# Kernel tuning notes

Hardware: AMD Instinct MI355X
Metric: run time of the kernel (lower is better)

## Reference

```python
import jax, jax.numpy as jnp
import numpy as np

V, N, D, HEADS = 4, 1536, 256, 4


def setup_inputs() -> dict:
    key = jax.random.key(0)
    ks = jax.random.split(key, 8)
    s = 0.05  # weight init scale
    return {
        "H": jax.random.normal(ks[0], (V, N, D), jnp.float32),
        "C": jax.random.normal(ks[1], (V, V, N, N), jnp.float32),
        "WQ": jax.random.normal(ks[2], (V, D, D), jnp.float32) * s,
        "WK": jax.random.normal(ks[3], (V, D, D), jnp.float32) * s,
        "WV": jax.random.normal(ks[4], (V, D, D), jnp.float32) * s,
        "in_proj_w": jax.random.normal(ks[5], (3 * D, D), jnp.float32) * s,
        "in_proj_b": jnp.zeros((3 * D,), jnp.float32),
        "out_proj_w": jax.random.normal(ks[6], (D, D), jnp.float32) * s,
        "out_proj_b": jnp.zeros((D,), jnp.float32),
        "alphas": jnp.full((V,), 0.95, jnp.float32),
        "alpha_align": jnp.asarray(0.5, jnp.float32),
        "beta": jnp.asarray(0.5, jnp.float32),
        "topk": 32,
    }


def _ircva(H, in_proj_w, in_proj_b, out_proj_w, out_proj_b, alphas):
    # torch MultiheadAttention, seq=V, batch=N, embed=D, heads=HEADS
    dh = D // HEADS
    qkv = jnp.einsum('snd,ed->sne', H, in_proj_w) + in_proj_b  # (V,N,3D)
    q, k, v = jnp.split(qkv, 3, axis=-1)
    q = q.reshape(V, N, HEADS, dh)
    k = k.reshape(V, N, HEADS, dh)
    v = v.reshape(V, N, HEADS, dh)
    att = jnp.einsum('snhd,tnhd->nhst', q, k) / jnp.sqrt(jnp.float32(dh))
    w = jax.nn.softmax(att, axis=-1)
    o = jnp.einsum('nhst,tnhd->snhd', w, v).reshape(V, N, D)
    fusion = jnp.einsum('snd,ed->sne', o, out_proj_w) + out_proj_b
    a = alphas[:, None, None]
    return fusion * a + (1.0 - a) * H  # (V,N,D)


def _crcva(aligned, C, WQ, WK, WV, K):
    # per-view projections: Linear y = x @ W.T
    Qn = jnp.einsum('vnd,ved->vne', aligned, WQ)
    Kn = jnp.einsum('vnd,ved->vne', aligned, WK)
    Vn = jnp.einsum('vnd,ved->vne', aligned, WV)
    # per-row top-k sparsification of C[p,q]
    vals, idx = jax.lax.top_k(C, K)  # (V,V,N,K)
    Cf = C.reshape(-1, N)
    rows = jnp.arange(Cf.shape[0])[:, None]
    sparse = jnp.zeros_like(Cf).at[rows, idx.reshape(-1, K)].set(vals.reshape(-1, K))
    sparse = sparse.reshape(V, V, N, N)
    row_sum = sparse.sum(axis=-1, keepdims=True) + 1e-12
    C_hat = sparse / row_sum
    # diagonal (p==q) pairs are left as zeros in the torch code
    offdiag = (1.0 - jnp.eye(V, dtype=C.dtype))[:, :, None, None]
    C_hat = C_hat * offdiag
    mask = (C_hat > 0).astype(C.dtype)
    scores = jnp.einsum('pnd,qmd->pqnm', Qn, Kn) / jnp.sqrt(jnp.float32(D))
    scores = scores * mask + (1.0 - mask) * (-1e9)
    alpha_nbr = jax.nn.softmax(scores, axis=-1)
    return jnp.einsum('pqnm,qmd->pnd', alpha_nbr, Vn)  # (V,N,D)


def reference(H, C, WQ, WK, WV, in_proj_w, in_proj_b, out_proj_w, out_proj_b,
              alphas, alpha_align, beta, topk):
    aligned = _ircva(H, in_proj_w, in_proj_b, out_proj_w, out_proj_b, alphas)
    nbr = _crcva(aligned, C, WQ, WK, WV, int(topk))
    a = jax.nn.sigmoid(alpha_align)
    f_fuse = jax.nn.relu(a * aligned + (1.0 - a) * nbr)
    return beta * H + (1.0 - beta) * f_fuse  # (V,N,D)
```

## Files before the change

### kernel.cpp

```cpp
#include <hip/hip_runtime.h>
#include <hip/hip_bf16.h>
#include <math.h>

typedef __bf16 bf16x8 __attribute__((ext_vector_type(8)));
typedef __bf16 bf16x4 __attribute__((ext_vector_type(4)));
typedef float  f32x4  __attribute__((ext_vector_type(4)));

static constexpr int kV = 4;
static constexpr int kN = 1536;
static constexpr int kD = 256;
static constexpr int kTopK = 32;

__global__ __launch_bounds__(256) void convert_kernel(
    const float* __restrict__ H, const float* __restrict__ inW,
    const float* __restrict__ outW, const float* __restrict__ WQ,
    const float* __restrict__ WK, const float* __restrict__ WV,
    __bf16* __restrict__ Hb, __bf16* __restrict__ inWb,
    __bf16* __restrict__ outWb, __bf16* __restrict__ Wqkvb,
    float* __restrict__ Vmean)
{
    if (blockIdx.x == 0) {
        f32x4 z = {0.f, 0.f, 0.f, 0.f};
        *(f32x4*)(Vmean + threadIdx.x * 4) = z;
    }
    int idx = (blockIdx.x * 256 + threadIdx.x) * 4;
    const float* src; __bf16* dst; int off;
    if      (idx < 1572864) { src = H;    dst = Hb;             off = idx; }
    else if (idx < 1769472) { src = inW;  dst = inWb;           off = idx - 1572864; }
    else if (idx < 1835008) { src = outW; dst = outWb;          off = idx - 1769472; }
    else if (idx < 2097152) { src = WQ;   dst = Wqkvb;          off = idx - 1835008; }
    else if (idx < 2359296) { src = WK;   dst = Wqkvb + 262144; off = idx - 2097152; }
    else                    { src = WV;   dst = Wqkvb + 524288; off = idx - 2359296; }
    f32x4 v = *(const f32x4*)(src + off);
    bf16x4 b;
#pragma unroll
    for (int j = 0; j < 4; ++j) b[j] = (__bf16)v[j];
    *(bf16x4*)(dst + off) = b;
}

__global__ __launch_bounds__(256) void gemm_qkv_kernel(
    const __bf16* __restrict__ A, const __bf16* __restrict__ Bm,
    const float* __restrict__ bias, __bf16* __restrict__ outB)
{
    const int Nc = 768, K = 256;
    int wave = blockIdx.x * 4 + (threadIdx.x >> 6);
    int tm  = wave / 12;
    int tn4 = wave - tm * 12;
    int lane = threadIdx.x & 63;
    int r    = lane & 15;
    int quad = lane >> 4;
    const __bf16* Ap = A + (size_t)(tm * 32 + r) * K + quad * 8;
    const __bf16* Bp = Bm + (size_t)(tn4 * 64 + r) * K + quad * 8;
    f32x4 acc[2][4] = {};
    for (int k0 = 0; k0 < K; k0 += 32) {
        bf16x8 a0 = *(const bf16x8*)(Ap + k0);
        bf16x8 a1 = *(const bf16x8*)(Ap + (size_t)16 * K + k0);
#pragma unroll
        for (int t = 0; t < 4; ++t) {
            bf16x8 b = *(const bf16x8*)(Bp + (size_t)t * 16 * K + k0);
            acc[0][t] = __builtin_amdgcn_mfma_f32_16x16x32_bf16(a0, b, acc[0][t], 0, 0, 0);
            acc[1][t] = __builtin_amdgcn_mfma_f32_16x16x32_bf16(a1, b, acc[1][t], 0, 0, 0);
        }
    }
#pragma unroll
    for (int t = 0; t < 4; ++t) {
        int gn = tn4 * 64 + t * 16 + r;
        float bv = bias[gn];
#pragma unroll
        for (int mt = 0; mt < 2; ++mt)
#pragma unroll
            for (int i = 0; i < 4; ++i) {
                int gm = tm * 32 + mt * 16 + quad * 4 + i;
                outB[(size_t)gm * Nc + gn] = (__bf16)(acc[mt][t][i] + bv);
            }
    }
}

__global__ __launch_bounds__(256) void attg3_kernel(
    const __bf16* __restrict__ qkv, const __bf16* __restrict__ outWb,
    const float* __restrict__ outBias, const float* __restrict__ H,
    const float* __restrict__ alphas,
    float* __restrict__ alignedF, __bf16* __restrict__ alignedB)
{
    __shared__ __bf16 obuf[16][280];
    int n0 = blockIdx.x * 4;
    int tid = threadIdx.x;
    int h = tid >> 6, d = tid & 63;
#pragma unroll
    for (int ni = 0; ni < 4; ++ni) {
        int n = n0 + ni;
        float q[4], k[4], vv[4];
#pragma unroll
        for (int s = 0; s < 4; ++s) {
            size_t base = (size_t)(s * kN + n) * 768 + h * 64 + d;
            q[s]  = (float)qkv[base];
            k[s]  = (float)qkv[base + 256];
            vv[s] = (float)qkv[base + 512];
        }
        float att[4][4];
#pragma unroll
        for (int s = 0; s < 4; ++s)
#pragma unroll
            for (int t = 0; t < 4; ++t) {
                float p = q[s] * k[t];
#pragma unroll
                for (int off = 32; off > 0; off >>= 1) p += __shfl_xor(p, off);
                att[s][t] = p * 0.125f;
            }
#pragma unroll
        for (int s = 0; s < 4; ++s) {
            float mx = fmaxf(fmaxf(att[s][0], att[s][1]), fmaxf(att[s][2], att[s][3]));
            float e0 = __expf(att[s][0] - mx), e1 = __expf(att[s][1] - mx);
            float e2 = __expf(att[s][2] - mx), e3 = __expf(att[s][3] - mx);
            float inv = 1.f / (e0 + e1 + e2 + e3);
            float ov = (e0 * vv[0] + e1 * vv[1] + e2 * vv[2] + e3 * vv[3]) * inv;
            obuf[s * 4 + ni][h * 64 + d] = (__bf16)ov;
        }
    }
    __syncthreads();
    int w = tid >> 6, lane = tid & 63;
    int r = lane & 15, quad = lane >> 4;
    f32x4 acc[4] = {};
    for (int k0 = 0; k0 < 256; k0 += 32) {
        bf16x8 a = *(const bf16x8*)&obuf[r][quad * 8 + k0];
#pragma unroll
        for (int t = 0; t < 4; ++t) {
            bf16x8 b = *(const bf16x8*)(outWb + (size_t)(w * 64 + t * 16 + r) * 256 + quad * 8 + k0);
            acc[t] = __builtin_amdgcn_mfma_f32_16x16x32_bf16(a, b, acc[t], 0, 0, 0);
        }
    }
#pragma unroll
    for (int t = 0; t < 4; ++t) {
        int gn = w * 64 + t * 16 + r;
        float bv = outBias[gn];
#pragma unroll
        for (int i = 0; i < 4; ++i) {
            int rl = quad * 4 + i;
            int s = rl >> 2, ni = rl & 3;
            size_t gr = (size_t)(s * kN + n0 + ni);
            float a_ = alphas[s];
            size_t off = gr * kD + gn;
            float res = a_ * (acc[t][i] + bv) + (1.f - a_) * H[off];
            alignedF[off] = res;
            alignedB[off] = (__bf16)res;
        }
    }
}

__global__ __launch_bounds__(256) void gemm_qkv3_kernel(
    const __bf16* __restrict__ A, const __bf16* __restrict__ W,
    __bf16* __restrict__ Qn, float* __restrict__ KnF, float* __restrict__ VnF,
    float* __restrict__ Vmean)
{
    int proj = blockIdx.y;
    const __bf16* Wb = W + (size_t)proj * 4 * 65536;
    int b = blockIdx.x;
    int view = b / 48;
    int tn4 = threadIdx.x >> 6;
    int lane = threadIdx.x & 63;
    int r = lane & 15, quad = lane >> 4;
    const __bf16* Ap = A + (size_t)(b * 32 + r) * kD + quad * 8;
    const __bf16* Bp = Wb + (size_t)view * 65536 + (size_t)(tn4 * 64 + r) * kD + quad * 8;
    f32x4 acc[2][4] = {};
    for (int k0 = 0; k0 < kD; k0 += 32) {
        bf16x8 a0 = *(const bf16x8*)(Ap + k0);
        bf16x8 a1 = *(const bf16x8*)(Ap + (size_t)16 * kD + k0);
#pragma unroll
        for (int t = 0; t < 4; ++t) {
            bf16x8 bb = *(const bf16x8*)(Bp + (size_t)t * 16 * kD + k0);
            acc[0][t] = __builtin_amdgcn_mfma_f32_16x16x32_bf16(a0, bb, acc[0][t], 0, 0, 0);
            acc[1][t] = __builtin_amdgcn_mfma_f32_16x16x32_bf16(a1, bb, acc[1][t], 0, 0, 0);
        }
    }
    float* OF = (proj == 1) ? KnF : VnF;
#pragma unroll
    for (int t = 0; t < 4; ++t) {
        int gn = tn4 * 64 + t * 16 + r;
#pragma unroll
        for (int mt = 0; mt < 2; ++mt)
#pragma unroll
            for (int i = 0; i < 4; ++i) {
                int gm = b * 32 + mt * 16 + quad * 4 + i;
                if (proj == 0) Qn[(size_t)gm * kD + gn] = (__bf16)acc[mt][t][i];
                else           OF[(size_t)gm * kD + gn] = acc[mt][t][i];
            }
    }
    if (proj == 2) {
#pragma unroll
        for (int t = 0; t < 4; ++t) {
            float cs = 0.f;
#pragma unroll
            for (int mt = 0; mt < 2; ++mt)
#pragma unroll
                for (int i = 0; i < 4; ++i) cs += acc[mt][t][i];
            cs += __shfl_xor(cs, 16);
            cs += __shfl_xor(cs, 32);
            if (quad == 0)
                atomicAdd(&Vmean[view * kD + tn4 * 64 + t * 16 + r], cs * (1.f / 1536.f));
        }
    }
}

__global__ __launch_bounds__(256) void crcva_kernel(
    const float* __restrict__ C,
    const __bf16* __restrict__ Qn, const float* __restrict__ KnF,
    const float* __restrict__ VnF, const float* __restrict__ Vmean,
    const float* __restrict__ alignedF, const float* __restrict__ H,
    const float* __restrict__ alpha_align, const float* __restrict__ beta,
    float* __restrict__ out)
{
    int gid = blockIdx.x;
    int j8  = gid & 7;
    int p   = j8 & 3;
    int n   = ((gid >> 3) << 1) | (j8 >> 2);
    int tid = threadIdx.x;
    int w = tid >> 6, lane = tid & 63;
    __shared__ unsigned int hist[3][257];
    __shared__ unsigned int sbin[3];
    __shared__ unsigned int idxl[3][kTopK];
    __shared__ unsigned int scnt[3];
    __shared__ unsigned int ckey[3][152];
    __shared__ unsigned int cidx[3][152];
    __shared__ float qsh[kD];
    __shared__ float wsh[96];
    __shared__ int   osh[96];
    __shared__ float part[4][kD];

    size_t eoff = ((size_t)p * kN + n) * kD + tid;
    float pre_al = alignedF[eoff];
    float pre_h  = H[eoff];
    float pre_vm = Vmean[p * kD + tid];
    float pre_aa = alpha_align[0];
    float pre_bt = beta[0];

    if (w < 3) {
        int q = w + (w >= p ? 1 : 0);
        const float* row = C + ((size_t)((p * kV + q) * kN + n)) * kN;
        unsigned int key[24];
#pragma unroll
        for (int j = 0; j < 6; ++j) {
            f32x4 v4 = __builtin_nontemporal_load((const f32x4*)(row + j * 256 + lane * 4));
#pragma unroll
            for (int e = 0; e < 4; ++e) {
                unsigned int u = __float_as_uint(v4[e]);
                key[j * 4 + e] = u ^ ((unsigned int)((int)u >> 31) | 0x80000000u);
            }
        }
        if (lane == 0) scnt[w] = 0;
        const unsigned int T0 = 0xBFCCCCCDu;
        unsigned int cand = 0;
#pragma unroll
        for (int j = 0; j < 24; ++j) cand |= (key[j] > T0) ? (1u << j) : 0u;
        unsigned int myc = (unsigned int)__popc(cand);
#pragma unroll
        for (int off = 1; off < 64; off <<= 1) myc += __shfl_xor(myc, off);
        bool fastsel = (myc >= kTopK && myc <= 150);
        unsigned int pref = 0, need = kTopK, h3win = 0;
        unsigned long long below = (1ull << lane) - 1ull;
        if (fastsel) {
            unsigned int ccnt = 0;
#pragma unroll
            for (int j = 0; j < 24; ++j) {
                bool b = (cand >> j) & 1u;
                unsigned long long m = __ballot(b);
                if (b) {
                    unsigned int pos = ccnt + (unsigned int)__popcll(m & below);
                    ckey[w][pos] = key[j];
                    cidx[w][pos] = (unsigned int)((j >> 2) * 256 + lane * 4 + (j & 3));
                }
                ccnt += (unsigned int)__popcll(m);
            }
            __builtin_amdgcn_wave_barrier();
#pragma unroll
            for (int pass = 0; pass < 4; ++pass) {
                const int shift = 24 - 8 * pass;
#pragma unroll
                for (int k2 = 0; k2 < 4; ++k2) hist[w][lane * 4 + k2] = 0;
                __builtin_amdgcn_wave_barrier();
#pragma unroll
                for (int s = 0; s < 3; ++s) {
                    int i = lane + s * 64;
                    if (i < (int)ccnt) {
                        unsigned int k = ckey[w][i];
                        if (pass == 0 || ((k ^ pref) >> (shift + 8)) == 0)
                            atomicAdd(&hist[w][(k >> shift) & 255u], 1u);
                    }
                }
                __builtin_amdgcn_wave_barrier();
                unsigned int h0 = hist[w][lane*4+0], h1 = hist[w][lane*4+1];
                unsigned int h2 = hist[w][lane*4+2], h3 = hist[w][lane*4+3];
                unsigned int s3 = h3, s2 = h2 + s3, s1 = h1 + s2, s0 = h0 + s1;
                unsigned int run = s0;
#pragma unroll
                for (int off = 1; off < 64; off <<= 1) {
                    unsigned int v = __shfl_down(run, off);
                    if (lane + off < 64) run += v;
                }
                unsigned int above = run - s0;
                unsigned int suf[4]  = {above+s0, above+s1, above+s2, above+s3};
                unsigned int sufN[4] = {above+s1, above+s2, above+s3, above};
#pragma unroll
                for (int k2 = 0; k2 < 4; ++k2)
                    if (suf[k2] >= need && sufN[k2] < need)
                        sbin[w] = ((unsigned int)(lane*4 + k2) << 22)
                                | ((suf[k2] - sufN[k2]) << 11) | sufN[k2];
                __builtin_amdgcn_wave_barrier();
                unsigned int pk = sbin[w];
                pref |= (pk >> 22) << shift;
                need -= (pk & 0x7FFu);
                if (pass == 3) h3win = (pk >> 11) & 0x7FFu;
                __builtin_amdgcn_wave_barrier();
            }
            unsigned int T = pref;
            if (h3win == need) {
#pragma unroll
                for (int s = 0; s < 3; ++s) {
                    int i = lane + s * 64;
                    if (i < (int)ccnt && ckey[w][i] >= T) {
                        unsigned int pos = atomicAdd(&scnt[w], 1u);
                        idxl[w][pos] = cidx[w][i];
                    }
                }
            } else {
                unsigned int eqBefore = 0;
                for (int j4 = 0; j4 < 6; ++j4) {
                    unsigned long long m[4];
#pragma unroll
                    for (int e = 0; e < 4; ++e)
                        m[e] = __ballot(((cand >> (j4*4+e)) & 1u) && key[j4*4+e] == T);
#pragma unroll
                    for (int e = 0; e < 4; ++e) {
                        unsigned int k = key[j4 * 4 + e];
                        bool inc = (cand >> (j4*4+e)) & 1u;
                        unsigned int rank = eqBefore;
#pragma unroll
                        for (int e2 = 0; e2 < 4; ++e2) rank += (unsigned int)__popcll(m[e2] & below);
                        for (int e2 = 0; e2 < e; ++e2) rank += (unsigned int)((m[e2] >> lane) & 1ull);
                        bool take = (inc && k > T) || (inc && k == T && rank < need);
                        if (take) {
                            unsigned int pos = atomicAdd(&scnt[w], 1u);
                            idxl[w][pos] = (unsigned int)(j4 * 256 + lane * 4 + e);
                        }
                    }
                    eqBefore += (unsigned int)(__popcll(m[0]) + __popcll(m[1])
                                             + __popcll(m[2]) + __popcll(m[3]));
                }
            }
        } else {
            if (myc < kTopK) {
                cand = 0;
#pragma unroll
                for (int j = 0; j < 24; ++j) cand |= (key[j] > 0x80000000u) ? (1u << j) : 0u;
            }
            need = kTopK;
#pragma unroll
            for (int pass = 0; pass < 4; ++pass) {
                const int shift = 24 - 8 * pass;
#pragma unroll
                for (int k2 = 0; k2 < 4; ++k2) hist[w][lane * 4 + k2] = 0;
                __builtin_amdgcn_wave_barrier();
#pragma unroll
                for (int j = 0; j < 24; ++j) {
                    unsigned int k = key[j];
                    bool match = ((cand >> j) & 1u) &&
                                 ((pass == 0) || (((k ^ pref) >> (shift + 8)) == 0));
                    if (match) atomicAdd(&hist[w][(k >> shift) & 255u], 1u);
                }
                __builtin_amdgcn_wave_barrier();
                unsigned int h0 = hist[w][lane*4+0], h1 = hist[w][lane*4+1];
                unsigned int h2 = hist[w][lane*4+2], h3 = hist[w][lane*4+3];
                unsigned int s3 = h3, s2 = h2 + s3, s1 = h1 + s2, s0 = h0 + s1;
                unsigned int run = s0;
#pragma unroll
                for (int off = 1; off < 64; off <<= 1) {
                    unsigned int v = __shfl_down(run, off);
                    if (lane + off < 64) run += v;
                }
                if (pass == 0) {
                    unsigned int tot = __shfl(run, 0);
                    need = need < tot ? need : tot;
                }
                unsigned int above = run - s0;
                unsigned int suf[4]  = {above+s0, above+s1, above+s2, above+s3};
                unsigned int sufN[4] = {above+s1, above+s2, above+s3, above};
#pragma unroll
                for (int k2 = 0; k2 < 4; ++k2)
                    if (suf[k2] >= need && sufN[k2] < need)
                        sbin[w] = ((unsigned int)(lane*4 + k2) << 22)
                                | ((suf[k2] - sufN[k2]) << 11) | sufN[k2];
                __builtin_amdgcn_wave_barrier();
                unsigned int pk = sbin[w];
                pref |= (pk >> 22) << shift;
                need -= (pk & 0x7FFu);
                if (pass == 3) h3win = (pk >> 11) & 0x7FFu;
                __builtin_amdgcn_wave_barrier();
            }
            unsigned int T = pref;
            if (h3win == need) {
#pragma unroll
                for (int j = 0; j < 24; ++j) {
                    if (((cand >> j) & 1u) && key[j] >= T) {
                        unsigned int pos = atomicAdd(&scnt[w], 1u);
                        idxl[w][pos] = (unsigned int)((j >> 2) * 256 + lane * 4 + (j & 3));
                    }
                }
            } else {
                unsigned int eqBefore = 0;
                for (int j4 = 0; j4 < 6; ++j4) {
                    unsigned long long m[4];
#pragma unroll
                    for (int e = 0; e < 4; ++e)
                        m[e] = __ballot(((cand >> (j4*4+e)) & 1u) && key[j4*4+e] == T);
#pragma unroll
                    for (int e = 0; e < 4; ++e) {
                        unsigned int k = key[j4 * 4 + e];
                        bool inc = (cand >> (j4*4+e)) & 1u;
                        unsigned int rank = eqBefore;
#pragma unroll
                        for (int e2 = 0; e2 < 4; ++e2) rank += (unsigned int)__popcll(m[e2] & below);
                        for (int e2 = 0; e2 < e; ++e2) rank += (unsigned int)((m[e2] >> lane) & 1ull);
                        bool take = (inc && k > T) || (inc && k == T && rank < need);
                        if (take) {
                            unsigned int pos = atomicAdd(&scnt[w], 1u);
                            idxl[w][pos] = (unsigned int)(j4 * 256 + lane * 4 + e);
                        }
                    }
                    eqBefore += (unsigned int)(__popcll(m[0]) + __popcll(m[1])
                                             + __popcll(m[2]) + __popcll(m[3]));
                }
            }
        }
    } else {
        bf16x4 qv = *(const bf16x4*)(Qn + ((size_t)p * kN + n) * kD + lane * 4);
#pragma unroll
        for (int e = 0; e < 4; ++e) qsh[lane * 4 + e] = (float)qv[e];
    }
    __syncthreads();

    if (tid < 192) {
        int j = tid >> 1, half = tid & 1;
        int g = j >> 5, r = j & 31;
        int q = g + (g >= p ? 1 : 0);
        int cnt = (int)scnt[g];
        bool valid = (r < cnt);
        int m = valid ? (int)idxl[g][r] : 0;
        int off = valid ? (q * kN + m) * kD : 0;
        float s = 0.f;
        if (valid) {
            const float* kr = KnF + off + half * 128;
            const float* qh = qsh + half * 128;
            float a0 = 0.f, a1 = 0.f, a2 = 0.f, a3 = 0.f;
#pragma unroll
            for (int dd = 0; dd < 128; dd += 16) {
                f32x4 k0 = *(const f32x4*)(kr + dd);
                f32x4 k1 = *(const f32x4*)(kr + dd + 4);
                f32x4 k2 = *(const f32x4*)(kr + dd + 8);
                f32x4 k3 = *(const f32x4*)(kr + dd + 12);
                const float* q0 = qh + dd;
                a0 += q0[0]*k0[0] + q0[1]*k0[1] + q0[2]*k0[2] + q0[3]*k0[3];
                a1 += q0[4]*k1[0] + q0[5]*k1[1] + q0[6]*k1[2] + q0[7]*k1[3];
                a2 += q0[8]*k2[0] + q0[9]*k2[1] + q0[10]*k2[2] + q0[11]*k2[3];
                a3 += q0[12]*k3[0] + q0[13]*k3[1] + q0[14]*k3[2] + q0[15]*k3[3];
            }
            s = (a0 + a1) + (a2 + a3);
        }
        s += __shfl_xor(s, 1);
        float sc = valid ? s * 0.0625f : -1e30f;
        float mx = sc;
#pragma unroll
        for (int o2 = 2; o2 <= 32; o2 <<= 1) mx = fmaxf(mx, __shfl_xor(mx, o2));
        float e = valid ? __expf(sc - mx) : 0.f;
        float ss = e;
#pragma unroll
        for (int o2 = 2; o2 <= 32; o2 <<= 1) ss += __shfl_xor(ss, o2);
        if (half == 0) {
            wsh[j] = (ss > 0.f) ? e / ss : 0.f;
            osh[j] = off;
        }
    }
    __syncthreads();

    {
        float a0 = 0.f, a1 = 0.f, a2 = 0.f, a3 = 0.f;
#pragma unroll
        for (int jj = 0; jj < 24; ++jj) {
            int j = w * 24 + jj;
            float wt = wsh[j];
            f32x4 v = *(const f32x4*)(VnF + osh[j] + lane * 4);
            a0 += wt * v[0]; a1 += wt * v[1]; a2 += wt * v[2]; a3 += wt * v[3];
        }
        f32x4 av = {a0, a1, a2, a3};
        *(f32x4*)&part[w][lane * 4] = av;
    }
    __syncthreads();

    float acc = pre_vm + part[0][tid] + part[1][tid] + part[2][tid] + part[3][tid];
    float aa = 1.f / (1.f + __expf(-pre_aa));
    float f  = fmaxf(aa * pre_al + (1.f - aa) * acc, 0.f);
    out[eoff] = pre_h * pre_bt + (1.f - pre_bt) * f;
}

extern "C" void kernel_launch(void* const* d_in, const int* in_sizes, int n_in,
                              void* d_out, int out_size, void* d_ws, size_t ws_size,
                              hipStream_t stream)
{
    const float* H        = (const float*)d_in[0];
    const float* C        = (const float*)d_in[1];
    const float* WQ       = (const float*)d_in[2];
    const float* WK       = (const float*)d_in[3];
    const float* WV       = (const float*)d_in[4];
    const float* inW      = (const float*)d_in[5];
    const float* inB      = (const float*)d_in[6];
    const float* outW     = (const float*)d_in[7];
    const float* outBias  = (const float*)d_in[8];
    const float* alphas   = (const float*)d_in[9];
    const float* alpha_al = (const float*)d_in[10];
    const float* beta     = (const float*)d_in[11];
    float* out = (float*)d_out;

    char* w = (char*)d_ws;
    __bf16* Hb       = (__bf16*)w;  w += (size_t)6144 * 256 * 2;
    __bf16* inWb     = (__bf16*)w;  w += (size_t)768 * 256 * 2;
    __bf16* outWb    = (__bf16*)w;  w += (size_t)256 * 256 * 2;
    __bf16* Wqkvb    = (__bf16*)w;  w += (size_t)3 * 4 * 256 * 256 * 2;
    __bf16* qkv      = (__bf16*)w;  w += (size_t)6144 * 768 * 2;
    __bf16* alignedB = (__bf16*)w;  w += (size_t)6144 * 256 * 2;
    float*  alignedF = (float*)w;   w += (size_t)6144 * 256 * 4;
    __bf16* Qn       = (__bf16*)w;  w += (size_t)6144 * 256 * 2;
    float*  KnF      = (float*)w;   w += (size_t)6144 * 256 * 4;
    float*  VnF      = (float*)w;   w += (size_t)6144 * 256 * 4;
    float*  Vmean    = (float*)w;   w += (size_t)4 * 256 * 4;

    convert_kernel<<<2560, 256, 0, stream>>>(H, inW, outW, WQ, WK, WV,
                                             Hb, inWb, outWb, Wqkvb, Vmean);
    gemm_qkv_kernel<<<576, 256, 0, stream>>>(Hb, inWb, inB, qkv);
    attg3_kernel<<<384, 256, 0, stream>>>(qkv, outWb, outBias, H, alphas,
                                          alignedF, alignedB);
    gemm_qkv3_kernel<<<dim3(192, 3), 256, 0, stream>>>(alignedB, Wqkvb,
                                                       Qn, KnF, VnF, Vmean);
    crcva_kernel<<<6144, 256, 0, stream>>>(C, Qn, KnF, VnF, Vmean,
        alignedF, H, alpha_al, beta, out);
}
```

Before: 431.3 us.

## Store K and V projections in bf16 and scope top-k key registers

The K and V projection outputs are now written as bf16 rather than fp32, so the sparse neighbour gather in crcva reads half the bytes per row. The V accumulation is reorganised so each half-wave loads 8 bf16 values and the two halves are combined with a shuffle. The top-k selection code is restructured so the key register array lives in a narrower scope, and the tie-handling slow path reloads the C row from memory instead of keeping the keys live, which may lower register pressure. In exchange, K and V lose precision, and the rare tie path pays for an extra global read.

Measured after the change: 347.5 us. 1.24x faster.

```diff
diff --git a/kernel.cpp b/kernel.cpp
--- a/kernel.cpp
+++ b/kernel.cpp
@@ -149,10 +149,11 @@
 
 __global__ __launch_bounds__(256) void gemm_qkv3_kernel(
     const __bf16* __restrict__ A, const __bf16* __restrict__ W,
-    __bf16* __restrict__ Qn, float* __restrict__ KnF, float* __restrict__ VnF,
+    __bf16* __restrict__ O0, __bf16* __restrict__ O1, __bf16* __restrict__ O2,
     float* __restrict__ Vmean)
 {
     int proj = blockIdx.y;
+    __bf16* Ob = (proj == 0) ? O0 : (proj == 1) ? O1 : O2;
     const __bf16* Wb = W + (size_t)proj * 4 * 65536;
     int b = blockIdx.x;
     int view = b / 48;
@@ -172,7 +173,6 @@
             acc[1][t] = __builtin_amdgcn_mfma_f32_16x16x32_bf16(a1, bb, acc[1][t], 0, 0, 0);
         }
     }
-    float* OF = (proj == 1) ? KnF : VnF;
 #pragma unroll
     for (int t = 0; t < 4; ++t) {
         int gn = tn4 * 64 + t * 16 + r;
@@ -181,8 +181,7 @@
 #pragma unroll
             for (int i = 0; i < 4; ++i) {
                 int gm = b * 32 + mt * 16 + quad * 4 + i;
-                if (proj == 0) Qn[(size_t)gm * kD + gn] = (__bf16)acc[mt][t][i];
-                else           OF[(size_t)gm * kD + gn] = acc[mt][t][i];
+                Ob[(size_t)gm * kD + gn] = (__bf16)acc[mt][t][i];
             }
     }
     if (proj == 2) {
@@ -203,8 +202,8 @@
 
 __global__ __launch_bounds__(256) void crcva_kernel(
     const float* __restrict__ C,
-    const __bf16* __restrict__ Qn, const float* __restrict__ KnF,
-    const float* __restrict__ VnF, const float* __restrict__ Vmean,
+    const __bf16* __restrict__ Qn, const __bf16* __restrict__ Kn,
+    const __bf16* __restrict__ Vn, const float* __restrict__ Vmean,
     const float* __restrict__ alignedF, const float* __restrict__ H,
     const float* __restrict__ alpha_align, const float* __restrict__ beta,
     float* __restrict__ out)
@@ -236,197 +235,203 @@
     if (w < 3) {
         int q = w + (w >= p ? 1 : 0);
         const float* row = C + ((size_t)((p * kV + q) * kN + n)) * kN;
-        unsigned int key[24];
-#pragma unroll
-        for (int j = 0; j < 6; ++j) {
-            f32x4 v4 = __builtin_nontemporal_load((const f32x4*)(row + j * 256 + lane * 4));
-#pragma unroll
-            for (int e = 0; e < 4; ++e) {
-                unsigned int u = __float_as_uint(v4[e]);
-                key[j * 4 + e] = u ^ ((unsigned int)((int)u >> 31) | 0x80000000u);
-            }
-        }
         if (lane == 0) scnt[w] = 0;
         const unsigned int T0 = 0xBFCCCCCDu;
-        unsigned int cand = 0;
-#pragma unroll
-        for (int j = 0; j < 24; ++j) cand |= (key[j] > T0) ? (1u << j) : 0u;
-        unsigned int myc = (unsigned int)__popc(cand);
-#pragma unroll
-        for (int off = 1; off < 64; off <<= 1) myc += __shfl_xor(myc, off);
-        bool fastsel = (myc >= kTopK && myc <= 150);
+        unsigned long long below = (1ull << lane) - 1ull;
         unsigned int pref = 0, need = kTopK, h3win = 0;
-        unsigned long long below = (1ull << lane) - 1ull;
-        if (fastsel) {
-            unsigned int ccnt = 0;
-#pragma unroll
-            for (int j = 0; j < 24; ++j) {
-                bool b = (cand >> j) & 1u;
-                unsigned long long m = __ballot(b);
-                if (b) {
-                    unsigned int pos = ccnt + (unsigned int)__popcll(m & below);
-                    ckey[w][pos] = key[j];
-                    cidx[w][pos] = (unsigned int)((j >> 2) * 256 + lane * 4 + (j & 3));
-                }
-                ccnt += (unsigned int)__popcll(m);
+        unsigned int cand, myc;
+        {
+            unsigned int key[24];
+#pragma unroll
+            for (int j = 0; j < 6; ++j) {
+                f32x4 v4 = __builtin_nontemporal_load((const f32x4*)(row + j * 256 + lane * 4));
+#pragma unroll
+                for (int e = 0; e < 4; ++e) {
+                    unsigned int u = __float_as_uint(v4[e]);
+                    key[j * 4 + e] = u ^ ((unsigned int)((int)u >> 31) | 0x80000000u);
+                }
             }
-            __builtin_amdgcn_wave_barrier();
-#pragma unroll
-            for (int pass = 0; pass < 4; ++pass) {
-                const int shift = 24 - 8 * pass;
-#pragma unroll
-                for (int k2 = 0; k2 < 4; ++k2) hist[w][lane * 4 + k2] = 0;
+            cand = 0;
+#pragma unroll
+            for (int j = 0; j < 24; ++j) cand |= (key[j] > T0) ? (1u << j) : 0u;
+            myc = (unsigned int)__popc(cand);
+#pragma unroll
+            for (int off = 1; off < 64; off <<= 1) myc += __shfl_xor(myc, off);
+            if (myc >= kTopK && myc <= 150) {
+                unsigned int ccnt = 0;
+#pragma unroll
+                for (int j = 0; j < 24; ++j) {
+                    bool b = (cand >> j) & 1u;
+                    unsigned long long m = __ballot(b);
+                    if (b) {
+                        unsigned int pos = ccnt + (unsigned int)__popcll(m & below);
+                        ckey[w][pos] = key[j];
+                        cidx[w][pos] = (unsigned int)((j >> 2) * 256 + lane * 4 + (j & 3));
+                    }
+                    ccnt += (unsigned int)__popcll(m);
+                }
                 __builtin_amdgcn_wave_barrier();
 #pragma unroll
-                for (int s = 0; s < 3; ++s) {
-                    int i = lane + s * 64;
-                    if (i < (int)ccnt) {
-                        unsigned int k = ckey[w][i];
-                        if (pass == 0 || ((k ^ pref) >> (shift + 8)) == 0)
-                            atomicAdd(&hist[w][(k >> shift) & 255u], 1u);
-                    }
-                }
-                __builtin_amdgcn_wave_barrier();
-                unsigned int h0 = hist[w][lane*4+0], h1 = hist[w][lane*4+1];
-                unsigned int h2 = hist[w][lane*4+2], h3 = hist[w][lane*4+3];
-                unsigned int s3 = h3, s2 = h2 + s3, s1 = h1 + s2, s0 = h0 + s1;
-                unsigned int run = s0;
-#pragma unroll
-                for (int off = 1; off < 64; off <<= 1) {
-                    unsigned int v = __shfl_down(run, off);
-                    if (lane + off < 64) run += v;
-                }
-                unsigned int above = run - s0;
-                unsigned int suf[4]  = {above+s0, above+s1, above+s2, above+s3};
-                unsigned int sufN[4] = {above+s1, above+s2, above+s3, above};
-#pragma unroll
-                for (int k2 = 0; k2 < 4; ++k2)
-                    if (suf[k2] >= need && sufN[k2] < need)
-                        sbin[w] = ((unsigned int)(lane*4 + k2) << 22)
-                                | ((suf[k2] - sufN[k2]) << 11) | sufN[k2];
-                __builtin_amdgcn_wave_barrier();
-                unsigned int pk = sbin[w];
-                pref |= (pk >> 22) << shift;
-                need -= (pk & 0x7FFu);
-                if (pass == 3) h3win = (pk >> 11) & 0x7FFu;
-                __builtin_amdgcn_wave_barrier();
-            }
-            unsigned int T = pref;
-            if (h3win == need) {
-#pragma unroll
-                for (int s = 0; s < 3; ++s) {
-                    int i = lane + s * 64;
-                    if (i < (int)ccnt && ckey[w][i] >= T) {
-                        unsigned int pos = atomicAdd(&scnt[w], 1u);
-                        idxl[w][pos] = cidx[w][i];
+                for (int pass = 0; pass < 4; ++pass) {
+                    const int shift = 24 - 8 * pass;
+#pragma unroll
+                    for (int k2 = 0; k2 < 4; ++k2) hist[w][lane * 4 + k2] = 0;
+                    __builtin_amdgcn_wave_barrier();
+#pragma unroll
+                    for (int s = 0; s < 3; ++s) {
+                        int i = lane + s * 64;
+                        if (i < (int)ccnt) {
+                            unsigned int k = ckey[w][i];
+                            if (pass == 0 || ((k ^ pref) >> (shift + 8)) == 0)
+                                atomicAdd(&hist[w][(k >> shift) & 255u], 1u);
+                        }
+                    }
+                    __builtin_amdgcn_wave_barrier();
+                    unsigned int h0 = hist[w][lane*4+0], h1 = hist[w][lane*4+1];
+                    unsigned int h2 = hist[w][lane*4+2], h3 = hist[w][lane*4+3];
+                    unsigned int s3 = h3, s2 = h2 + s3, s1 = h1 + s2, s0 = h0 + s1;
+                    unsigned int run = s0;
+#pragma unroll
+                    for (int off = 1; off < 64; off <<= 1) {
+                        unsigned int v = __shfl_down(run, off);
+                        if (lane + off < 64) run += v;
+                    }
+                    unsigned int above = run - s0;
+                    unsigned int suf[4]  = {above+s0, above+s1, above+s2, above+s3};
+                    unsigned int sufN[4] = {above+s1, above+s2, above+s3, above};
+#pragma unroll
+                    for (int k2 = 0; k2 < 4; ++k2)
+                        if (suf[k2] >= need && sufN[k2] < need)
+                            sbin[w] = ((unsigned int)(lane*4 + k2) << 22)
+                                    | ((suf[k2] - sufN[k2]) << 11) | sufN[k2];
+                    __builtin_amdgcn_wave_barrier();
+                    unsigned int pk = sbin[w];
+                    pref |= (pk >> 22) << shift;
+                    need -= (pk & 0x7FFu);
+                    if (pass == 3) h3win = (pk >> 11) & 0x7FFu;
+                    __builtin_amdgcn_wave_barrier();
+                }
+                unsigned int T = pref;
+                if (h3win == need) {
+#pragma unroll
+                    for (int s = 0; s < 3; ++s) {
+                        int i = lane + s * 64;
+                        if (i < (int)ccnt && ckey[w][i] >= T) {
+                            unsigned int pos = atomicAdd(&scnt[w], 1u);
+                            idxl[w][pos] = cidx[w][i];
+                        }
+                    }
+                } else {
+                    unsigned int eqBefore = 0;
+                    for (int j4 = 0; j4 < 6; ++j4) {
+                        unsigned int k4[4];
+                        f32x4 v4 = *(const f32x4*)(row + j4 * 256 + lane * 4);
+#pragma unroll
+                        for (int e = 0; e < 4; ++e) {
+                            unsigned int u = __float_as_uint(v4[e]);
+                            k4[e] = u ^ ((unsigned int)((int)u >> 31) | 0x80000000u);
+                        }
+                        unsigned long long m[4];
+#pragma unroll
+                        for (int e = 0; e < 4; ++e) m[e] = __ballot(k4[e] == T);
+#pragma unroll
+                        for (int e = 0; e < 4; ++e) {
+                            unsigned int k = k4[e];
+                            unsigned int rank = eqBefore;
+#pragma unroll
+                            for (int e2 = 0; e2 < 4; ++e2) rank += (unsigned int)__popcll(m[e2] & below);
+                            for (int e2 = 0; e2 < e; ++e2) rank += (unsigned int)((m[e2] >> lane) & 1ull);
+                            bool take = (k > T) || (k == T && rank < need);
+                            if (take) {
+                                unsigned int pos = atomicAdd(&scnt[w], 1u);
+                                idxl[w][pos] = (unsigned int)(j4 * 256 + lane * 4 + e);
+                            }
+                        }
+                        eqBefore += (unsigned int)(__popcll(m[0]) + __popcll(m[1])
+                                                 + __popcll(m[2]) + __popcll(m[3]));
                     }
                 }
             } else {
-                unsigned int eqBefore = 0;
-                for (int j4 = 0; j4 < 6; ++j4) {
-                    unsigned long long m[4];
-#pragma unroll
-                    for (int e = 0; e < 4; ++e)
-                        m[e] = __ballot(((cand >> (j4*4+e)) & 1u) && key[j4*4+e] == T);
-#pragma unroll
-                    for (int e = 0; e < 4; ++e) {
-                        unsigned int k = key[j4 * 4 + e];
-                        bool inc = (cand >> (j4*4+e)) & 1u;
-                        unsigned int rank = eqBefore;
-#pragma unroll
-                        for (int e2 = 0; e2 < 4; ++e2) rank += (unsigned int)__popcll(m[e2] & below);
-                        for (int e2 = 0; e2 < e; ++e2) rank += (unsigned int)((m[e2] >> lane) & 1ull);
-                        bool take = (inc && k > T) || (inc && k == T && rank < need);
-                        if (take) {
+                if (myc < kTopK) {
+                    cand = 0;
+#pragma unroll
+                    for (int j = 0; j < 24; ++j) cand |= (key[j] > 0x80000000u) ? (1u << j) : 0u;
+                }
+#pragma unroll
+                for (int pass = 0; pass < 4; ++pass) {
+                    const int shift = 24 - 8 * pass;
+#pragma unroll
+                    for (int k2 = 0; k2 < 4; ++k2) hist[w][lane * 4 + k2] = 0;
+                    __builtin_amdgcn_wave_barrier();
+#pragma unroll
+                    for (int j = 0; j < 24; ++j) {
+                        unsigned int k = key[j];
+                        bool match = ((cand >> j) & 1u) &&
+                                     ((pass == 0) || (((k ^ pref) >> (shift + 8)) == 0));
+                        if (match) atomicAdd(&hist[w][(k >> shift) & 255u], 1u);
+                    }
+                    __builtin_amdgcn_wave_barrier();
+                    unsigned int h0 = hist[w][lane*4+0], h1 = hist[w][lane*4+1];
+                    unsigned int h2 = hist[w][lane*4+2], h3 = hist[w][lane*4+3];
+                    unsigned int s3 = h3, s2 = h2 + s3, s1 = h1 + s2, s0 = h0 + s1;
+                    unsigned int run = s0;
+#pragma unroll
+                    for (int off = 1; off < 64; off <<= 1) {
+                        unsigned int v = __shfl_down(run, off);
+                        if (lane + off < 64) run += v;
+                    }
+                    if (pass == 0) {
+                        unsigned int tot = __shfl(run, 0);
+                        need = need < tot ? need : tot;
+                    }
+                    unsigned int above = run - s0;
+                    unsigned int suf[4]  = {above+s0, above+s1, above+s2, above+s3};
+                    unsigned int sufN[4] = {above+s1, above+s2, above+s3, above};
+#pragma unroll
+                    for (int k2 = 0; k2 < 4; ++k2)
+                        if (suf[k2] >= need && sufN[k2] < need)
+                            sbin[w] = ((unsigned int)(lane*4 + k2) << 22)
+                                    | ((suf[k2] - sufN[k2]) << 11) | sufN[k2];
+                    __builtin_amdgcn_wave_barrier();
+                    unsigned int pk = sbin[w];
+                    pref |= (pk >> 22) << shift;
+                    need -= (pk & 0x7FFu);
+                    if (pass == 3) h3win = (pk >> 11) & 0x7FFu;
+                    __builtin_amdgcn_wave_barrier();
+                }
+                unsigned int T = pref;
+                if (h3win == need) {
+#pragma unroll
+                    for (int j = 0; j < 24; ++j) {
+                        if (((cand >> j) & 1u) && key[j] >= T) {
                             unsigned int pos = atomicAdd(&scnt[w], 1u);
-                            idxl[w][pos] = (unsigned int)(j4 * 256 + lane * 4 + e);
+                            idxl[w][pos] = (unsigned int)((j >> 2) * 256 + lane * 4 + (j & 3));
                         }
                     }
-                    eqBefore += (unsigned int)(__popcll(m[0]) + __popcll(m[1])
-                                             + __popcll(m[2]) + __popcll(m[3]));
-                }
-            }
-        } else {
-            if (myc < kTopK) {
-                cand = 0;
-#pragma unroll
-                for (int j = 0; j < 24; ++j) cand |= (key[j] > 0x80000000u) ? (1u << j) : 0u;
-            }
-            need = kTopK;
-#pragma unroll
-            for (int pass = 0; pass < 4; ++pass) {
-                const int shift = 24 - 8 * pass;
-#pragma unroll
-                for (int k2 = 0; k2 < 4; ++k2) hist[w][lane * 4 + k2] = 0;
-                __builtin_amdgcn_wave_barrier();
-#pragma unroll
-                for (int j = 0; j < 24; ++j) {
-                    unsigned int k = key[j];
-                    bool match = ((cand >> j) & 1u) &&
-                                 ((pass == 0) || (((k ^ pref) >> (shift + 8)) == 0));
-                    if (match) atomicAdd(&hist[w][(k >> shift) & 255u], 1u);
-                }
-                __builtin_amdgcn_wave_barrier();
-                unsigned int h0 = hist[w][lane*4+0], h1 = hist[w][lane*4+1];
-                unsigned int h2 = hist[w][lane*4+2], h3 = hist[w][lane*4+3];
-                unsigned int s3 = h3, s2 = h2 + s3, s1 = h1 + s2, s0 = h0 + s1;
-                unsigned int run = s0;
-#pragma unroll
-                for (int off = 1; off < 64; off <<= 1) {
-                    unsigned int v = __shfl_down(run, off);
-                    if (lane + off < 64) run += v;
-                }
-                if (pass == 0) {
-                    unsigned int tot = __shfl(run, 0);
-                    need = need < tot ? need : tot;
-                }
-                unsigned int above = run - s0;
-                unsigned int suf[4]  = {above+s0, above+s1, above+s2, above+s3};
-                unsigned int sufN[4] = {above+s1, above+s2, above+s3, above};
-#pragma unroll
-                for (int k2 = 0; k2 < 4; ++k2)
-                    if (suf[k2] >= need && sufN[k2] < need)
-                        sbin[w] = ((unsigned int)(lane*4 + k2) << 22)
-                                | ((suf[k2] - sufN[k2]) << 11) | sufN[k2];
-                __builtin_amdgcn_wave_barrier();
-                unsigned int pk = sbin[w];
-                pref |= (pk >> 22) << shift;
-                need -= (pk & 0x7FFu);
-                if (pass == 3) h3win = (pk >> 11) & 0x7FFu;
-                __builtin_amdgcn_wave_barrier();
-            }
-            unsigned int T = pref;
-            if (h3win == need) {
-#pragma unroll
-                for (int j = 0; j < 24; ++j) {
-                    if (((cand >> j) & 1u) && key[j] >= T) {
-                        unsigned int pos = atomicAdd(&scnt[w], 1u);
-                        idxl[w][pos] = (unsigned int)((j >> 2) * 256 + lane * 4 + (j & 3));
-                    }
-                }
-            } else {
-                unsigned int eqBefore = 0;
-                for (int j4 = 0; j4 < 6; ++j4) {
-                    unsigned long long m[4];
-#pragma unroll
-                    for (int e = 0; e < 4; ++e)
-                        m[e] = __ballot(((cand >> (j4*4+e)) & 1u) && key[j4*4+e] == T);
-#pragma unroll
-                    for (int e = 0; e < 4; ++e) {
-                        unsigned int k = key[j4 * 4 + e];
-                        bool inc = (cand >> (j4*4+e)) & 1u;
-                        unsigned int rank = eqBefore;
-#pragma unroll
-                        for (int e2 = 0; e2 < 4; ++e2) rank += (unsigned int)__popcll(m[e2] & below);
-                        for (int e2 = 0; e2 < e; ++e2) rank += (unsigned int)((m[e2] >> lane) & 1ull);
-                        bool take = (inc && k > T) || (inc && k == T && rank < need);
-                        if (take) {
-                            unsigned int pos = atomicAdd(&scnt[w], 1u);
-                            idxl[w][pos] = (unsigned int)(j4 * 256 + lane * 4 + e);
+                } else {
+                    unsigned int eqBefore = 0;
+                    for (int j4 = 0; j4 < 6; ++j4) {
+                        unsigned long long m[4];
+#pragma unroll
+                        for (int e = 0; e < 4; ++e)
+                            m[e] = __ballot(((cand >> (j4*4+e)) & 1u) && key[j4*4+e] == T);
+#pragma unroll
+                        for (int e = 0; e < 4; ++e) {
+                            unsigned int k = key[j4 * 4 + e];
+                            bool inc = (cand >> (j4*4+e)) & 1u;
+                            unsigned int rank = eqBefore;
+#pragma unroll
+                            for (int e2 = 0; e2 < 4; ++e2) rank += (unsigned int)__popcll(m[e2] & below);
+                            for (int e2 = 0; e2 < e; ++e2) rank += (unsigned int)((m[e2] >> lane) & 1ull);
+                            bool take = (inc && k > T) || (inc && k == T && rank < need);
+                            if (take) {
+                                unsigned int pos = atomicAdd(&scnt[w], 1u);
+                                idxl[w][pos] = (unsigned int)(j4 * 256 + lane * 4 + e);
+                            }
                         }
-                    }
-                    eqBefore += (unsigned int)(__popcll(m[0]) + __popcll(m[1])
-                                             + __popcll(m[2]) + __popcll(m[3]));
+                        eqBefore += (unsigned int)(__popcll(m[0]) + __popcll(m[1])
+                                                 + __popcll(m[2]) + __popcll(m[3]));
+                    }
                 }
             }
         }
@@ -447,20 +452,23 @@
         int off = valid ? (q * kN + m) * kD : 0;
         float s = 0.f;
         if (valid) {
-            const float* kr = KnF + off + half * 128;
-            const float* qh = qsh + half * 128;
+            const __bf16* kr = Kn + off + half * 128;
+            const float*  qh = qsh + half * 128;
             float a0 = 0.f, a1 = 0.f, a2 = 0.f, a3 = 0.f;
 #pragma unroll
-            for (int dd = 0; dd < 128; dd += 16) {
-                f32x4 k0 = *(const f32x4*)(kr + dd);
-                f32x4 k1 = *(const f32x4*)(kr + dd + 4);
-                f32x4 k2 = *(const f32x4*)(kr + dd + 8);
-                f32x4 k3 = *(const f32x4*)(kr + dd + 12);
+            for (int dd = 0; dd < 128; dd += 32) {
+                bf16x8 k0 = *(const bf16x8*)(kr + dd);
+                bf16x8 k1 = *(const bf16x8*)(kr + dd + 8);
+                bf16x8 k2 = *(const bf16x8*)(kr + dd + 16);
+                bf16x8 k3 = *(const bf16x8*)(kr + dd + 24);
                 const float* q0 = qh + dd;
-                a0 += q0[0]*k0[0] + q0[1]*k0[1] + q0[2]*k0[2] + q0[3]*k0[3];
-                a1 += q0[4]*k1[0] + q0[5]*k1[1] + q0[6]*k1[2] + q0[7]*k1[3];
-                a2 += q0[8]*k2[0] + q0[9]*k2[1] + q0[10]*k2[2] + q0[11]*k2[3];
-                a3 += q0[12]*k3[0] + q0[13]*k3[1] + q0[14]*k3[2] + q0[15]*k3[3];
+#pragma unroll
+                for (int e = 0; e < 8; ++e) {
+                    a0 += q0[e]      * (float)k0[e];
+                    a1 += q0[e + 8]  * (float)k1[e];
+                    a2 += q0[e + 16] * (float)k2[e];
+                    a3 += q0[e + 24] * (float)k3[e];
+                }
             }
             s = (a0 + a1) + (a2 + a3);
         }
@@ -481,16 +489,22 @@
     __syncthreads();
 
     {
-        float a0 = 0.f, a1 = 0.f, a2 = 0.f, a3 = 0.f;
-#pragma unroll
-        for (int jj = 0; jj < 24; ++jj) {
-            int j = w * 24 + jj;
+        int half32 = lane >> 5, l32 = lane & 31;
+        float a[8] = {};
+#pragma unroll
+        for (int it = 0; it < 12; ++it) {
+            int j = w * 24 + it * 2 + half32;
             float wt = wsh[j];
-            f32x4 v = *(const f32x4*)(VnF + osh[j] + lane * 4);
-            a0 += wt * v[0]; a1 += wt * v[1]; a2 += wt * v[2]; a3 += wt * v[3];
-        }
-        f32x4 av = {a0, a1, a2, a3};
-        *(f32x4*)&part[w][lane * 4] = av;
+            bf16x8 v = *(const bf16x8*)(Vn + osh[j] + l32 * 8);
+#pragma unroll
+            for (int e = 0; e < 8; ++e) a[e] += wt * (float)v[e];
+        }
+#pragma unroll
+        for (int e = 0; e < 8; ++e) a[e] += __shfl_xor(a[e], 32);
+        if (half32 == 0) {
+#pragma unroll
+            for (int e = 0; e < 8; ++e) part[w][l32 * 8 + e] = a[e];
+        }
     }
     __syncthreads();
 
@@ -527,8 +541,8 @@
     __bf16* alignedB = (__bf16*)w;  w += (size_t)6144 * 256 * 2;
     float*  alignedF = (float*)w;   w += (size_t)6144 * 256 * 4;
     __bf16* Qn       = (__bf16*)w;  w += (size_t)6144 * 256 * 2;
-    float*  KnF      = (float*)w;   w += (size_t)6144 * 256 * 4;
-    float*  VnF      = (float*)w;   w += (size_t)6144 * 256 * 4;
+    __bf16* Kn       = (__bf16*)w;  w += (size_t)6144 * 256 * 2;
+    __bf16* Vn       = (__bf16*)w;  w += (size_t)6144 * 256 * 2;
     float*  Vmean    = (float*)w;   w += (size_t)4 * 256 * 4;
 
     convert_kernel<<<2560, 256, 0, stream>>>(H, inW, outW, WQ, WK, WV,
@@ -537,7 +551,7 @@
     attg3_kernel<<<384, 256, 0, stream>>>(qkv, outWb, outBias, H, alphas,
                                           alignedF, alignedB);
     gemm_qkv3_kernel<<<dim3(192, 3), 256, 0, stream>>>(alignedB, Wqkvb,
-                                                       Qn, KnF, VnF, Vmean);
-    crcva_kernel<<<6144, 256, 0, stream>>>(C, Qn, KnF, VnF, Vmean,
+                                                       Qn, Kn, Vn, Vmean);
+    crcva_kernel<<<6144, 256, 0, stream>>>(C, Qn, Kn, Vn, Vmean,
         alignedF, H, alpha_al, beta, out);
 }
```
